# Kernel optimization log

Hardware: AMD Instinct MI355X
Metric: run time of the kernel (lower is better)

The kernel has to match this reference:

```python
import jax, jax.numpy as jnp
import numpy as np

N_NODES = 50000
N_EDGES = 1_000_000
D = 256


def gcn_conv(x, src, dst, ew, W, b, n):
    # PyG GCNConv with edge_weight: linear transform, add self-loops (w=1),
    # symmetric normalization deg^{-1/2} w deg^{-1/2}, scatter-sum, + bias.
    x = x @ W  # (n, out)
    loop = jnp.arange(n)
    src_l = jnp.concatenate([src, loop])
    dst_l = jnp.concatenate([dst, loop])
    ew_l = jnp.concatenate([ew, jnp.ones((n,), ew.dtype)])
    deg = jax.ops.segment_sum(ew_l, dst_l, num_segments=n)
    dinv = jnp.where(deg > 0, jax.lax.rsqrt(deg), 0.0).astype(x.dtype)
    norm = dinv[src_l] * ew_l * dinv[dst_l]  # (E+n,)
    out = jax.ops.segment_sum(norm[:, None] * x[src_l], dst_l, num_segments=n)
    return out + b


def setup_inputs() -> dict:
    key = jax.random.key(0)
    k = jax.random.split(key, 8)
    glorot = 1.0 / np.sqrt(D)
    return {
        "x": jax.random.normal(k[0], (N_NODES, D), jnp.float32),
        "edge_index": jax.random.randint(k[1], (2, N_EDGES), 0, N_NODES, jnp.int64),
        "edge_weight": jax.random.uniform(k[2], (N_EDGES,), jnp.float32),
        "W1": jax.random.normal(k[3], (D, D), jnp.float32) * glorot,
        "b1": jnp.zeros((D,), jnp.float32),
        "W2": jax.random.normal(k[4], (D, D), jnp.float32) * glorot,
        "b2": jnp.zeros((D,), jnp.float32),
    }


def reference(x, edge_index, edge_weight, W1, b1, W2, b2):
    n = x.shape[0]
    src, dst = edge_index[0], edge_index[1]
    h = gcn_conv(x, src, dst, edge_weight, W1, b1, n)
    h = jax.nn.relu(h)  # dropout is identity at eval
    out = gcn_conv(h, src, dst, edge_weight, W2, b2, n)
    return out
```

## Files before the change

kernel.cpp:

```cpp
#include <hip/hip_runtime.h>
#include <hip/hip_bf16.h>
#include <stdint.h>


#define D 256
#define SCAN_B 512

typedef __attribute__((ext_vector_type(8))) short short8;
typedef __attribute__((ext_vector_type(4))) float floatx4;

__device__ inline unsigned short f2bf_rne(float f) {
    union { float f; uint32_t u; } v; v.f = f;
    uint32_t u = v.u;
    return (unsigned short)((u + 0x7FFFu + ((u >> 16) & 1u)) >> 16);
}
__device__ inline float bf_lo(uint32_t u) { union { uint32_t u; float f; } v; v.u = u << 16; return v.f; }
__device__ inline float bf_hi(uint32_t u) { union { uint32_t u; float f; } v; v.u = u & 0xFFFF0000u; return v.f; }

#define FXS 16777216.0f

__global__ void pass1_kernel(const int* __restrict__ dst, const float* __restrict__ ew,
                             unsigned long long* __restrict__ packed,
                             int* __restrict__ rank, int E) {
    int e = blockIdx.x * 256 + threadIdx.x;
    if (e < E) {
        int d = dst[e];
        uint32_t fx = __float2uint_rn(ew[e] * FXS);
        unsigned long long old =
            atomicAdd(&packed[d], ((unsigned long long)fx << 32) | 1ull);
        rank[e] = (int)(uint32_t)old;
    }
}

__global__ void unpack_kernel(const unsigned long long* __restrict__ packed,
                              int* __restrict__ counts, float* __restrict__ dinv, int n) {
    int i = blockIdx.x * 256 + threadIdx.x;
    if (i < n) {
        unsigned long long p = packed[i];
        counts[i] = (int)(uint32_t)p;
        float deg = (float)(p >> 32) * (1.0f / FXS) + 1.0f;
        dinv[i] = rsqrtf(deg);
    }
}

__global__ void scan1_kernel(const int* __restrict__ counts, int* __restrict__ row_start,
                             int* __restrict__ blockSums, int n) {
    __shared__ int s[SCAN_B];
    int t = threadIdx.x;
    int gid = blockIdx.x * SCAN_B + t;
    int v = (gid < n) ? counts[gid] : 0;
    s[t] = v;
    __syncthreads();
    for (int off = 1; off < SCAN_B; off <<= 1) {
        int add = (t >= off) ? s[t - off] : 0;
        __syncthreads();
        s[t] += add;
        __syncthreads();
    }
    if (gid < n) row_start[gid] = s[t] - v;
    if (t == SCAN_B - 1) blockSums[blockIdx.x] = s[SCAN_B - 1];
}

__global__ void scan2_kernel(const int* __restrict__ blockSums, int* __restrict__ blockOffsets, int nb) {
    __shared__ int s[128];
    int t = threadIdx.x;
    int v = (t < nb) ? blockSums[t] : 0;
    s[t] = v;
    __syncthreads();
    for (int off = 1; off < 128; off <<= 1) {
        int add = (t >= off) ? s[t - off] : 0;
        __syncthreads();
        s[t] += add;
        __syncthreads();
    }
    if (t < nb) blockOffsets[t] = s[t] - v;
}

__global__ void scan3_kernel(int* __restrict__ row_start,
                             const int* __restrict__ blockOffsets, int n, int E) {
    int gid = blockIdx.x * SCAN_B + threadIdx.x;
    if (gid < n) row_start[gid] += blockOffsets[blockIdx.x];
    if (gid == 0) row_start[n] = E;
}

__global__ void fill_kernel(const int* __restrict__ src, const int* __restrict__ dst,
                            const float* __restrict__ ew, const int* __restrict__ rank,
                            const int* __restrict__ row_start, const float* __restrict__ dinv,
                            int* __restrict__ esrc, float* __restrict__ ecoef, int E) {
    int e = blockIdx.x * 256 + threadIdx.x;
    if (e < E) {
        int s = src[e], d = dst[e];
        int pos = row_start[d] + rank[e];
        esrc[pos] = s;
        ecoef[pos] = dinv[s] * ew[e] * dinv[d];
    }
}

__global__ void cvt_x_kernel(const float* __restrict__ in, uint32_t* __restrict__ out, int n2) {
    int i = blockIdx.x * 256 + threadIdx.x;
    if (i < n2) {
        float2 f = ((const float2*)in)[i];
        out[i] = (uint32_t)f2bf_rne(f.x) | ((uint32_t)f2bf_rne(f.y) << 16);
    }
}

__global__ __launch_bounds__(1024) void cvt_wT_kernel(const float* __restrict__ W,
                                                      unsigned short* __restrict__ Wt) {
    __shared__ float s[32][33];
    int k0 = blockIdx.y * 32, n0 = blockIdx.x * 32;
    int tx = threadIdx.x, ty = threadIdx.y;
    s[ty][tx] = W[(k0 + ty) * D + n0 + tx];
    __syncthreads();
    Wt[(n0 + ty) * D + k0 + tx] = f2bf_rne(s[tx][ty]);
}

#define GBM 128
#define GBN 128
#define GBK 32
#define LDA 40

__global__ __launch_bounds__(256) void gemm_bf16_kernel(const unsigned short* __restrict__ A,
                                                        const unsigned short* __restrict__ Bt,
                                                        unsigned short* __restrict__ C, int n) {
    __shared__ unsigned short As[GBM][LDA];
    __shared__ unsigned short Bs[GBN][LDA];
    int t = threadIdx.x;
    int bm = blockIdx.x * GBM;
    int bn = blockIdx.y * GBN;
    int w = t >> 6, l = t & 63;
    int wm = (w >> 1) * 64, wn = (w & 1) * 64;
    int lr = l & 15;
    int lq = l >> 4;
    floatx4 acc[4][4] = {};
    for (int k0 = 0; k0 < D; k0 += GBK) {
        #pragma unroll
        for (int i = 0; i < 2; i++) {
            int c = t + i * 256;
            int row = c >> 2;
            int kk = (c & 3) * 8;
            int gr = bm + row;
            short8 av = {};
            if (gr < n) av = *(const short8*)&A[(size_t)gr * D + k0 + kk];
            *(short8*)&As[row][kk] = av;
            short8 bv = *(const short8*)&Bt[(size_t)(bn + row) * D + k0 + kk];
            *(short8*)&Bs[row][kk] = bv;
        }
        __syncthreads();
        short8 af[4], bfr[4];
        #pragma unroll
        for (int i = 0; i < 4; i++) af[i] = *(const short8*)&As[wm + i * 16 + lr][lq * 8];
        #pragma unroll
        for (int j = 0; j < 4; j++) bfr[j] = *(const short8*)&Bs[wn + j * 16 + lr][lq * 8];
        #pragma unroll
        for (int i = 0; i < 4; i++)
            #pragma unroll
            for (int j = 0; j < 4; j++)
                acc[i][j] = __builtin_amdgcn_mfma_f32_16x16x32_bf16(af[i], bfr[j], acc[i][j], 0, 0, 0);
        __syncthreads();
    }
    #pragma unroll
    for (int i = 0; i < 4; i++) {
        #pragma unroll
        for (int r = 0; r < 4; r++) {
            int row = bm + wm + i * 16 + lq * 4 + r;
            if (row >= n) continue;
            #pragma unroll
            for (int j = 0; j < 4; j++) {
                int col = bn + wn + j * 16 + lr;
                C[(size_t)row * D + col] = f2bf_rne(acc[i][j][r]);
            }
        }
    }
}

template <bool RELU, bool OUT_BF16>
__global__ __launch_bounds__(128) void gather_kernel(const uint32_t* __restrict__ xwb,
                                                     const int* __restrict__ row_start,
                                                     const int* __restrict__ esrc,
                                                     const float* __restrict__ ecoef,
                                                     const float* __restrict__ dinv,
                                                     const float* __restrict__ bias,
                                                     void* __restrict__ outv) {
    int i = blockIdx.x;
    int t = threadIdx.x;
    float di = dinv[i];
    float ws = di * di;
    uint32_t u0 = xwb[(size_t)i * 128 + t];
    float2 bb = ((const float2*)bias)[t];
    float2 a0, a1;
    a0.x = ws * bf_lo(u0) + bb.x;
    a0.y = ws * bf_hi(u0) + bb.y;
    a1.x = 0.0f; a1.y = 0.0f;
    int beg = row_start[i], end = row_start[i + 1];
    int j = beg;
    for (; j + 2 <= end; j += 2) {
        int   s0 = esrc[j],     s1 = esrc[j + 1];
        float c0 = ecoef[j],    c1 = ecoef[j + 1];
        uint32_t v0 = xwb[(size_t)s0 * 128 + t];
        uint32_t v1 = xwb[(size_t)s1 * 128 + t];
        a0.x += c0 * bf_lo(v0); a0.y += c0 * bf_hi(v0);
        a1.x += c1 * bf_lo(v1); a1.y += c1 * bf_hi(v1);
    }
    if (j < end) {
        int s0 = esrc[j];
        float c0 = ecoef[j];
        uint32_t v0 = xwb[(size_t)s0 * 128 + t];
        a0.x += c0 * bf_lo(v0); a0.y += c0 * bf_hi(v0);
    }
    float2 acc;
    acc.x = a0.x + a1.x;
    acc.y = a0.y + a1.y;
    if (RELU) {
        acc.x = fmaxf(acc.x, 0.0f);
        acc.y = fmaxf(acc.y, 0.0f);
    }
    if (OUT_BF16) {
        ((uint32_t*)outv)[(size_t)i * 128 + t] =
            (uint32_t)f2bf_rne(acc.x) | ((uint32_t)f2bf_rne(acc.y) << 16);
    } else {
        ((float2*)outv)[(size_t)i * 128 + t] = acc;
    }
}

extern "C" void kernel_launch(void* const* d_in, const int* in_sizes, int n_in,
                              void* d_out, int out_size, void* d_ws, size_t ws_size,
                              hipStream_t stream) {
    const float* x  = (const float*)d_in[0];
    const int*   ei = (const int*)d_in[1];
    const float* ew = (const float*)d_in[2];
    const float* W1 = (const float*)d_in[3];
    const float* b1 = (const float*)d_in[4];
    const float* W2 = (const float*)d_in[5];
    const float* b2 = (const float*)d_in[6];
    float* out = (float*)d_out;

    const int n = in_sizes[0] / D;
    const int E = in_sizes[2];
    const int* src = ei;
    const int* dst = ei + E;

    char* ws = (char*)d_ws;
    size_t off = 0;
    auto carve = [&](size_t bytes) {
        char* p = ws + off;
        off = (off + bytes + 255) & ~(size_t)255;
        return p;
    };
    unsigned long long* packed = (unsigned long long*)carve((size_t)n * 8);
    float* dinv        = (float*)carve((size_t)n * 4);
    int*   counts      = (int*)carve((size_t)n * 4);
    int*   row_start   = (int*)carve((size_t)(n + 1) * 4);
    int*   blockSums   = (int*)carve(128 * 4);
    int*   blockOffsets= (int*)carve(128 * 4);
    int*   rank        = (int*)carve((size_t)E * 4);
    int*   esrc        = (int*)carve((size_t)E * 4);
    float* ecoef       = (float*)carve((size_t)E * 4);
    unsigned short* xb  = (unsigned short*)carve((size_t)n * D * 2);
    unsigned short* w1t = (unsigned short*)carve((size_t)D * D * 2);
    unsigned short* w2t = (unsigned short*)carve((size_t)D * D * 2);
    unsigned short* xwb = (unsigned short*)carve((size_t)n * D * 2);
    unsigned short* hb  = (unsigned short*)carve((size_t)n * D * 2);

    const int nb_scan = (n + SCAN_B - 1) / SCAN_B;
    const int nb_edge = (E + 255) / 256;
    const int nb_node = (n + 255) / 256;

    hipMemsetAsync(packed, 0, (size_t)n * 8, stream);

    pass1_kernel<<<nb_edge, 256, 0, stream>>>(dst, ew, packed, rank, E);
    unpack_kernel<<<nb_node, 256, 0, stream>>>(packed, counts, dinv, n);
    scan1_kernel<<<nb_scan, SCAN_B, 0, stream>>>(counts, row_start, blockSums, n);
    scan2_kernel<<<1, 128, 0, stream>>>(blockSums, blockOffsets, nb_scan);
    scan3_kernel<<<nb_scan, SCAN_B, 0, stream>>>(row_start, blockOffsets, n, E);
    fill_kernel<<<nb_edge, 256, 0, stream>>>(src, dst, ew, rank, row_start, dinv, esrc, ecoef, E);

    int n2 = n * D / 2;
    cvt_x_kernel<<<(n2 + 255) / 256, 256, 0, stream>>>(x, (uint32_t*)xb, n2);
    cvt_wT_kernel<<<dim3(8, 8), dim3(32, 32), 0, stream>>>(W1, w1t);
    cvt_wT_kernel<<<dim3(8, 8), dim3(32, 32), 0, stream>>>(W2, w2t);

    dim3 ggrid((n + GBM - 1) / GBM, D / GBN);
    gemm_bf16_kernel<<<ggrid, 256, 0, stream>>>(xb, w1t, xwb, n);
    gather_kernel<true, true><<<n, 128, 0, stream>>>((const uint32_t*)xwb, row_start, esrc, ecoef,
                                                     dinv, b1, hb);
    gemm_bf16_kernel<<<ggrid, 256, 0, stream>>>(hb, w2t, xwb, n);
    gather_kernel<false, false><<<n, 128, 0, stream>>>((const uint32_t*)xwb, row_start, esrc, ecoef,
                                                       dinv, b2, out);
}
```

Baseline: 405.9 us.

## Fuse x conversion into GEMM, merge weight transposes, widen gather to wave-per-node

Converts fp32 x to bf16 inside the first GEMM's tile load, which removes the separate cvt_x kernel and its bf16 copy of x. The two weight-transpose launches are merged into one by using grid z. The gather kernel now maps one 64-lane wavefront to each node, four nodes per block, with 8-byte loads and four edges in flight per iteration, clamping indices and zeroing coefficients at the row tail. The aim is fewer launches, less intermediate traffic and more memory-level parallelism in the gather, at the cost of fp32 reads of x in the GEMM being redone for each N tile.

New measurement: 386.8 us. 4.7% less time.

```diff
diff --git a/kernel.cpp b/kernel.cpp
--- a/kernel.cpp
+++ b/kernel.cpp
@@ -96,17 +96,13 @@
     }
 }
 
-__global__ void cvt_x_kernel(const float* __restrict__ in, uint32_t* __restrict__ out, int n2) {
-    int i = blockIdx.x * 256 + threadIdx.x;
-    if (i < n2) {
-        float2 f = ((const float2*)in)[i];
-        out[i] = (uint32_t)f2bf_rne(f.x) | ((uint32_t)f2bf_rne(f.y) << 16);
-    }
-}
-
-__global__ __launch_bounds__(1024) void cvt_wT_kernel(const float* __restrict__ W,
-                                                      unsigned short* __restrict__ Wt) {
+__global__ __launch_bounds__(1024) void cvt_wT_kernel(const float* __restrict__ Wa,
+                                                      const float* __restrict__ Wb,
+                                                      unsigned short* __restrict__ Wta,
+                                                      unsigned short* __restrict__ Wtb) {
     __shared__ float s[32][33];
+    const float* W = blockIdx.z ? Wb : Wa;
+    unsigned short* Wt = blockIdx.z ? Wtb : Wta;
     int k0 = blockIdx.y * 32, n0 = blockIdx.x * 32;
     int tx = threadIdx.x, ty = threadIdx.y;
     s[ty][tx] = W[(k0 + ty) * D + n0 + tx];
@@ -119,7 +115,8 @@
 #define GBK 32
 #define LDA 40
 
-__global__ __launch_bounds__(256) void gemm_bf16_kernel(const unsigned short* __restrict__ A,
+template <bool AFP32>
+__global__ __launch_bounds__(256) void gemm_bf16_kernel(const void* __restrict__ Ap,
                                                         const unsigned short* __restrict__ Bt,
                                                         unsigned short* __restrict__ C, int n) {
     __shared__ unsigned short As[GBM][LDA];
@@ -140,7 +137,19 @@
             int kk = (c & 3) * 8;
             int gr = bm + row;
             short8 av = {};
-            if (gr < n) av = *(const short8*)&A[(size_t)gr * D + k0 + kk];
+            if (gr < n) {
+                if (AFP32) {
+                    const float* ap = (const float*)Ap + (size_t)gr * D + k0 + kk;
+                    float4 f0 = *(const float4*)ap;
+                    float4 f1 = *(const float4*)(ap + 4);
+                    av[0] = (short)f2bf_rne(f0.x); av[1] = (short)f2bf_rne(f0.y);
+                    av[2] = (short)f2bf_rne(f0.z); av[3] = (short)f2bf_rne(f0.w);
+                    av[4] = (short)f2bf_rne(f1.x); av[5] = (short)f2bf_rne(f1.y);
+                    av[6] = (short)f2bf_rne(f1.z); av[7] = (short)f2bf_rne(f1.w);
+                } else {
+                    av = *(const short8*)((const unsigned short*)Ap + (size_t)gr * D + k0 + kk);
+                }
+            }
             *(short8*)&As[row][kk] = av;
             short8 bv = *(const short8*)&Bt[(size_t)(bn + row) * D + k0 + kk];
             *(short8*)&Bs[row][kk] = bv;
@@ -174,51 +183,57 @@
 }
 
 template <bool RELU, bool OUT_BF16>
-__global__ __launch_bounds__(128) void gather_kernel(const uint32_t* __restrict__ xwb,
+__global__ __launch_bounds__(256) void gather_kernel(const uint2* __restrict__ xwb,
                                                      const int* __restrict__ row_start,
                                                      const int* __restrict__ esrc,
                                                      const float* __restrict__ ecoef,
                                                      const float* __restrict__ dinv,
                                                      const float* __restrict__ bias,
-                                                     void* __restrict__ outv) {
-    int i = blockIdx.x;
-    int t = threadIdx.x;
+                                                     void* __restrict__ outv, int n) {
+    int lane = threadIdx.x & 63;
+    int i = __builtin_amdgcn_readfirstlane((blockIdx.x << 2) + (threadIdx.x >> 6));
+    if (i >= n) return;
     float di = dinv[i];
     float ws = di * di;
-    uint32_t u0 = xwb[(size_t)i * 128 + t];
-    float2 bb = ((const float2*)bias)[t];
-    float2 a0, a1;
-    a0.x = ws * bf_lo(u0) + bb.x;
-    a0.y = ws * bf_hi(u0) + bb.y;
-    a1.x = 0.0f; a1.y = 0.0f;
+    uint2 u0 = xwb[(size_t)i * 64 + lane];
+    float4 bb = ((const float4*)bias)[lane];
+    float a0 = ws * bf_lo(u0.x) + bb.x;
+    float a1 = ws * bf_hi(u0.x) + bb.y;
+    float a2 = ws * bf_lo(u0.y) + bb.z;
+    float a3 = ws * bf_hi(u0.y) + bb.w;
     int beg = row_start[i], end = row_start[i + 1];
-    int j = beg;
-    for (; j + 2 <= end; j += 2) {
-        int   s0 = esrc[j],     s1 = esrc[j + 1];
-        float c0 = ecoef[j],    c1 = ecoef[j + 1];
-        uint32_t v0 = xwb[(size_t)s0 * 128 + t];
-        uint32_t v1 = xwb[(size_t)s1 * 128 + t];
-        a0.x += c0 * bf_lo(v0); a0.y += c0 * bf_hi(v0);
-        a1.x += c1 * bf_lo(v1); a1.y += c1 * bf_hi(v1);
-    }
-    if (j < end) {
-        int s0 = esrc[j];
+    for (int j = beg; j < end; j += 4) {
+        int e1 = min(j + 1, end - 1), e2 = min(j + 2, end - 1), e3 = min(j + 3, end - 1);
+        int s0 = esrc[j], s1 = esrc[e1], s2 = esrc[e2], s3 = esrc[e3];
         float c0 = ecoef[j];
-        uint32_t v0 = xwb[(size_t)s0 * 128 + t];
-        a0.x += c0 * bf_lo(v0); a0.y += c0 * bf_hi(v0);
-    }
-    float2 acc;
-    acc.x = a0.x + a1.x;
-    acc.y = a0.y + a1.y;
+        float c1 = (j + 1 < end) ? ecoef[e1] : 0.0f;
+        float c2 = (j + 2 < end) ? ecoef[e2] : 0.0f;
+        float c3 = (j + 3 < end) ? ecoef[e3] : 0.0f;
+        uint2 v0 = xwb[(size_t)s0 * 64 + lane];
+        uint2 v1 = xwb[(size_t)s1 * 64 + lane];
+        uint2 v2 = xwb[(size_t)s2 * 64 + lane];
+        uint2 v3 = xwb[(size_t)s3 * 64 + lane];
+        a0 += c0 * bf_lo(v0.x); a1 += c0 * bf_hi(v0.x);
+        a2 += c0 * bf_lo(v0.y); a3 += c0 * bf_hi(v0.y);
+        a0 += c1 * bf_lo(v1.x); a1 += c1 * bf_hi(v1.x);
+        a2 += c1 * bf_lo(v1.y); a3 += c1 * bf_hi(v1.y);
+        a0 += c2 * bf_lo(v2.x); a1 += c2 * bf_hi(v2.x);
+        a2 += c2 * bf_lo(v2.y); a3 += c2 * bf_hi(v2.y);
+        a0 += c3 * bf_lo(v3.x); a1 += c3 * bf_hi(v3.x);
+        a2 += c3 * bf_lo(v3.y); a3 += c3 * bf_hi(v3.y);
+    }
     if (RELU) {
-        acc.x = fmaxf(acc.x, 0.0f);
-        acc.y = fmaxf(acc.y, 0.0f);
+        a0 = fmaxf(a0, 0.0f); a1 = fmaxf(a1, 0.0f);
+        a2 = fmaxf(a2, 0.0f); a3 = fmaxf(a3, 0.0f);
     }
     if (OUT_BF16) {
-        ((uint32_t*)outv)[(size_t)i * 128 + t] =
-            (uint32_t)f2bf_rne(acc.x) | ((uint32_t)f2bf_rne(acc.y) << 16);
+        uint2 o;
+        o.x = (uint32_t)f2bf_rne(a0) | ((uint32_t)f2bf_rne(a1) << 16);
+        o.y = (uint32_t)f2bf_rne(a2) | ((uint32_t)f2bf_rne(a3) << 16);
+        ((uint2*)outv)[(size_t)i * 64 + lane] = o;
     } else {
-        ((float2*)outv)[(size_t)i * 128 + t] = acc;
+        float4 o; o.x = a0; o.y = a1; o.z = a2; o.w = a3;
+        ((float4*)outv)[(size_t)i * 64 + lane] = o;
     }
 }
 
@@ -255,7 +270,6 @@
     int*   rank        = (int*)carve((size_t)E * 4);
     int*   esrc        = (int*)carve((size_t)E * 4);
     float* ecoef       = (float*)carve((size_t)E * 4);
-    unsigned short* xb  = (unsigned short*)carve((size_t)n * D * 2);
     unsigned short* w1t = (unsigned short*)carve((size_t)D * D * 2);
     unsigned short* w2t = (unsigned short*)carve((size_t)D * D * 2);
     unsigned short* xwb = (unsigned short*)carve((size_t)n * D * 2);
@@ -274,16 +288,14 @@
     scan3_kernel<<<nb_scan, SCAN_B, 0, stream>>>(row_start, blockOffsets, n, E);
     fill_kernel<<<nb_edge, 256, 0, stream>>>(src, dst, ew, rank, row_start, dinv, esrc, ecoef, E);
 
-    int n2 = n * D / 2;
-    cvt_x_kernel<<<(n2 + 255) / 256, 256, 0, stream>>>(x, (uint32_t*)xb, n2);
-    cvt_wT_kernel<<<dim3(8, 8), dim3(32, 32), 0, stream>>>(W1, w1t);
-    cvt_wT_kernel<<<dim3(8, 8), dim3(32, 32), 0, stream>>>(W2, w2t);
+    cvt_wT_kernel<<<dim3(8, 8, 2), dim3(32, 32), 0, stream>>>(W1, W2, w1t, w2t);
 
     dim3 ggrid((n + GBM - 1) / GBM, D / GBN);
-    gemm_bf16_kernel<<<ggrid, 256, 0, stream>>>(xb, w1t, xwb, n);
-    gather_kernel<true, true><<<n, 128, 0, stream>>>((const uint32_t*)xwb, row_start, esrc, ecoef,
-                                                     dinv, b1, hb);
-    gemm_bf16_kernel<<<ggrid, 256, 0, stream>>>(hb, w2t, xwb, n);
-    gather_kernel<false, false><<<n, 128, 0, stream>>>((const uint32_t*)xwb, row_start, esrc, ecoef,
-                                                       dinv, b2, out);
-}
+    dim3 agrid((n + 3) / 4);
+    gemm_bf16_kernel<true><<<ggrid, 256, 0, stream>>>(x, w1t, xwb, n);
+    gather_kernel<true, true><<<agrid, 256, 0, stream>>>((const uint2*)xwb, row_start, esrc, ecoef,
+                                                         dinv, b1, hb, n);
+    gemm_bf16_kernel<false><<<ggrid, 256, 0, stream>>>(hb, w2t, xwb, n);
+    gather_kernel<false, false><<<agrid, 256, 0, stream>>>((const uint2*)xwb, row_start, esrc, ecoef,
+                                                           dinv, b2, out, n);
+}
```
